# Kernel tuning notes

Measured on AMD Instinct MI355X. Metric: run time of the kernel, lower is better.

## Reference

```python
import jax, jax.numpy as jnp
import numpy as np

N = 16384      # number of nodes (pos rows)
S = 16384      # number of src nodes (src_pos rows)
E = 262144     # number of edges (COO entries)
D = 512        # embed_dim
H = 8          # num_heads
HD = D // H    # head_dim = 64
HID = 1024     # mlp hidden
MLP_IN = D + 3 * H  # 536
EPS = 1e-5


def layer_norm(x, g, b):
    mu = jnp.mean(x, axis=-1, keepdims=True)
    var = jnp.mean((x - mu) ** 2, axis=-1, keepdims=True)
    return (x - mu) * jax.lax.rsqrt(var + EPS) * g + b


def setup_inputs() -> dict:
    key = jax.random.key(0)
    ks = jax.random.split(key, 20)
    s = 1.0 / np.sqrt(D)
    sh = 1.0 / np.sqrt(HID)
    return {
        "x": jax.random.normal(ks[0], (N, D), jnp.float32),
        "Wq": jax.random.uniform(ks[1], (D, D), jnp.float32, -s, s),
        "bq": jnp.zeros((D,), jnp.float32),
        "Wk": jax.random.uniform(ks[2], (D, D), jnp.float32, -s, s),
        "bk": jnp.zeros((D,), jnp.float32),
        "g_att": jnp.ones((D,), jnp.float32),
        "b_att": jnp.zeros((D,), jnp.float32),
        "g_mlp": jnp.ones((D,), jnp.float32),
        "b_mlp": jnp.zeros((D,), jnp.float32),
        "W_in": jax.random.uniform(ks[3], (HID, MLP_IN), jnp.float32, -s, s),
        "b_in": jnp.zeros((HID,), jnp.float32),
        "W_out": jax.random.uniform(ks[4], (D, HID), jnp.float32, -sh, sh),
        "b_out": jnp.zeros((D,), jnp.float32),
        "att_bias": jax.random.normal(ks[5], (H, E), jnp.float32),
        "dist": jax.random.uniform(ks[6], (E,), jnp.float32, 0.5, 6.0),
        "pos": jax.random.normal(ks[7], (N, 3), jnp.float32),
        "src_pos": jax.random.normal(ks[8], (S, 3), jnp.float32),
        "row_index": jax.random.randint(ks[9], (E,), 0, N),
        "src_index": jax.random.randint(ks[10], (E,), 0, S),
        "org_to_src": jax.random.randint(ks[11], (S,), 0, N),
    }


def reference(x, Wq, bq, Wk, bk, g_att, b_att, g_mlp, b_mlp, W_in, b_in,
              W_out, b_out, att_bias, dist, pos, src_pos,
              row_index, src_index, org_to_src):
    n = x.shape[0]
    z = layer_norm(x, g_att, b_att)
    q = (z @ Wq.T + bq).reshape(n, H, HD)          # [N,H,hd]
    k = (z @ Wk.T + bk).reshape(n, H, HD)          # [N,H,hd]
    k_src = k[org_to_src]                          # [S,H,hd]
    # per-edge masked logits: q[row] . k_src[col] / sqrt(hd) + bias
    qe = q[row_index]                              # [E,H,hd]
    ke = k_src[src_index]                          # [E,H,hd]
    logits = jnp.einsum('ehd,ehd->eh', qe, ke) / jnp.sqrt(jnp.float32(HD))
    logits = logits + att_bias.T                   # [E,H]
    # segment (per-row) softmax over incident edges
    m = jax.ops.segment_max(logits, row_index, num_segments=n)
    p = jnp.exp(logits - m[row_index])
    den = jax.ops.segment_sum(p, row_index, num_segments=n)
    att = p / den[row_index]                       # [E,H]
    inv = jnp.where(dist == 0, 0.0, 1.0 / dist)[:, None]
    att = att * inv
    # sparse bmm: feat[h,row] += att * src_pos[col]; rowsum for centering
    sp = src_pos[src_index]                        # [E,3]
    feat = jax.ops.segment_sum(att[:, :, None] * sp[:, None, :],
                               row_index, num_segments=n)   # [N,H,3]
    rowsum = jax.ops.segment_sum(att, row_index, num_segments=n)  # [N,H]
    feat = feat - rowsum[:, :, None] * pos[:, None, :]
    feat = feat.reshape(n, H * 3)
    z2 = layer_norm(x, g_mlp, b_mlp)
    h = jax.nn.gelu(jnp.concatenate([z2, feat], axis=-1) @ W_in.T + b_in)
    return x + (h @ W_out.T + b_out)
```

## Files before the change

### kernel.cpp

```cpp
#include <hip/hip_runtime.h>
#include <math.h>


typedef unsigned short u16;
typedef __attribute__((ext_vector_type(8))) short bf16x8;
typedef __attribute__((ext_vector_type(4))) float f32x4;
typedef __attribute__((ext_vector_type(2))) float f32x2;

constexpr int N_NODES = 16384;
constexpr int E_EDGES = 262144;
constexpr int D = 512;
constexpr int KIN = 544;

constexpr size_t OFF_ZATT = 0;
constexpr size_t OFF_ZCAT = 16777216;
constexpr size_t OFF_WQK  = 34603008;
constexpr size_t OFF_BQK  = 35651584;
constexpr size_t OFF_WIN  = 35655680;
constexpr size_t OFF_WOUT = 36769792;
constexpr size_t OFF_QK   = 37818368;
constexpr size_t OFF_CNT  = 54595584;
constexpr size_t OFF_BKT  = 54661120;
constexpr size_t OFF_ATT  = 58855424;
constexpr size_t OFF_HBF  = 107548672;

static __device__ __forceinline__ u16 f2bf(float f) {
  union { float f; unsigned int u; } v; v.f = f;
  unsigned int u = v.u;
  u = u + 0x7FFFu + ((u >> 16) & 1u);
  return (u16)(u >> 16);
}
static __device__ __forceinline__ void gload16(const u16* g, u16* l) {
  __builtin_amdgcn_global_load_lds(
      (const __attribute__((address_space(1))) unsigned int*)g,
      (__attribute__((address_space(3))) unsigned int*)l, 16, 0, 0);
}

__global__ __launch_bounds__(256) void prep_weights(
    const float* __restrict__ Wq, const float* __restrict__ Wk,
    const float* __restrict__ bq, const float* __restrict__ bk,
    const float* __restrict__ W_in, const float* __restrict__ W_out,
    u16* __restrict__ wqk, float* __restrict__ bqk,
    u16* __restrict__ win, u16* __restrict__ wout)
{
  const int gid = blockIdx.x * 256 + threadIdx.x;
  if (gid < 512 * 1024) {
    wqk[gid]  = f2bf(gid < 512 * 512 ? Wq[gid] : Wk[gid - 512 * 512]);
    wout[gid] = f2bf(W_out[gid]);
  }
  if (gid < 1024 * 544) {
    const int r = gid / 544, c = gid - r * 544;
    win[gid] = f2bf(c < 536 ? W_in[r * 536 + c] : 0.f);
  }
  if (gid < 1024) bqk[gid] = gid < 512 ? bq[gid] : bk[gid - 512];
}

__global__ __launch_bounds__(256) void ln_kernel(
    const float* __restrict__ x,
    const float* __restrict__ g1, const float* __restrict__ b1,
    const float* __restrict__ g2, const float* __restrict__ b2,
    u16* __restrict__ zatt, u16* __restrict__ zcat)
{
  const int row = blockIdx.x;
  const int t = threadIdx.x;
  const float2 v = *(const float2*)(x + (size_t)row * D + t * 2);
  float s = v.x + v.y;
  float s2 = v.x * v.x + v.y * v.y;
#pragma unroll
  for (int m = 1; m < 64; m <<= 1) {
    s  += __shfl_xor(s, m, 64);
    s2 += __shfl_xor(s2, m, 64);
  }
  __shared__ float red[8];
  const int wv = t >> 6;
  if ((t & 63) == 0) { red[wv] = s; red[4 + wv] = s2; }
  __syncthreads();
  s  = red[0] + red[1] + red[2] + red[3];
  s2 = red[4] + red[5] + red[6] + red[7];
  const float mu = s * (1.f / D);
  const float var = s2 * (1.f / D) - mu * mu;
  const float rs = rsqrtf(var + 1e-5f);
  const int c0 = t * 2;
  const float n0 = (v.x - mu) * rs, n1 = (v.y - mu) * rs;
  zatt[(size_t)row * D + c0]       = f2bf(n0 * g1[c0] + b1[c0]);
  zatt[(size_t)row * D + c0 + 1]   = f2bf(n1 * g1[c0 + 1] + b1[c0 + 1]);
  zcat[(size_t)row * KIN + c0]     = f2bf(n0 * g2[c0] + b2[c0]);
  zcat[(size_t)row * KIN + c0 + 1] = f2bf(n1 * g2[c0 + 1] + b2[c0 + 1]);
  if (t < 32) zcat[(size_t)row * KIN + D + t] = 0;
}

__global__ __launch_bounds__(256) void scatter_kernel(
    const int* __restrict__ row_index, int* __restrict__ cnt, int* __restrict__ bucket)
{
  const int gid = blockIdx.x * 256 + threadIdx.x;
  const int r = row_index[gid];
  const int p = atomicAdd(&cnt[r], 1);
  if (p < 64) bucket[(size_t)r * 64 + p] = gid;
}

__global__ __launch_bounds__(256) void tbias_kernel(
    const float* __restrict__ att_bias, float* __restrict__ attT)
{
  const int e = blockIdx.x * 256 + threadIdx.x;
  float v[8];
#pragma unroll
  for (int h = 0; h < 8; ++h) v[h] = att_bias[(size_t)h * E_EDGES + e];
  float* out = attT + (size_t)e * 8;
  *(float4*)out       = *(float4*)&v[0];
  *(float4*)(out + 4) = *(float4*)&v[4];
}

template <int EPI, int WPE>
__global__ __launch_bounds__(256, WPE) void gemm_nt(
    const u16* __restrict__ A, const u16* __restrict__ B,
    const float* __restrict__ bias, const float* __restrict__ resid,
    void* __restrict__ Cout, int M, int Nn, int K)
{
  constexpr int BM = 128, BN = 128, BK = 32;
  __shared__ __align__(16) u16 As[BM * BK];
  __shared__ __align__(16) u16 Bs[BN * BK];
  const int tid = threadIdx.x;
  const int lane = tid & 63;
  const int wave = tid >> 6;
  const int m0 = blockIdx.x * BM;
  const int n0 = blockIdx.y * BN;
  const int wm = (wave >> 1) * 64;
  const int wn = (wave & 1) * 64;
  const int fr = lane & 15;
  const int fq = lane >> 4;
  const int srow = lane >> 2;
  const int skoff = (lane & 3) * 8;

  f32x4 acc[4][4];
#pragma unroll
  for (int i = 0; i < 4; ++i)
#pragma unroll
    for (int j = 0; j < 4; ++j) acc[i][j] = 0.f;

  for (int k0 = 0; k0 < K; k0 += BK) {
    __syncthreads();
#pragma unroll
    for (int r = 0; r < 2; ++r) {
      const int rowbase = r * 64 + wave * 16;
      gload16(A + (size_t)(m0 + rowbase + srow) * K + k0 + skoff, As + rowbase * BK);
      gload16(B + (size_t)(n0 + rowbase + srow) * K + k0 + skoff, Bs + rowbase * BK);
    }
    __syncthreads();
    bf16x8 af[4], bfr[4];
#pragma unroll
    for (int mi = 0; mi < 4; ++mi)
      af[mi] = *(const bf16x8*)(As + (wm + mi * 16 + fr) * BK + fq * 8);
#pragma unroll
    for (int ni = 0; ni < 4; ++ni)
      bfr[ni] = *(const bf16x8*)(Bs + (wn + ni * 16 + fr) * BK + fq * 8);
#pragma unroll
    for (int mi = 0; mi < 4; ++mi)
#pragma unroll
      for (int ni = 0; ni < 4; ++ni)
        acc[mi][ni] = __builtin_amdgcn_mfma_f32_16x16x32_bf16(af[mi], bfr[ni], acc[mi][ni], 0, 0, 0);
  }

#pragma unroll
  for (int mi = 0; mi < 4; ++mi) {
#pragma unroll
    for (int ni = 0; ni < 4; ++ni) {
      const int col = n0 + wn + ni * 16 + fr;
      const float bv = bias[col];
#pragma unroll
      for (int rr = 0; rr < 4; ++rr) {
        const int row = m0 + wm + mi * 16 + fq * 4 + rr;
        float v = acc[mi][ni][rr] + bv;
        if (EPI == 1) {
          const float nu = -1.5957691216057308f * (v + 0.044715f * v * v * v);
          const float sg = __builtin_amdgcn_rcpf(1.f + __expf(nu));
          ((u16*)Cout)[(size_t)row * Nn + col] = f2bf(v * sg);
        } else if (EPI == 2) {
          ((float*)Cout)[(size_t)row * Nn + col] = v + resid[(size_t)row * Nn + col];
        } else {
          const int pk = __builtin_amdgcn_cvt_pk_fp8_f32(v, v, 0, false);
          ((unsigned char*)Cout)[(size_t)row * Nn + col] = (unsigned char)(pk & 0xFF);
        }
      }
    }
  }
}

__global__ __launch_bounds__(256) void edge_csr(
    const unsigned char* __restrict__ qk8, const float* __restrict__ attT,
    const float* __restrict__ dist, const float* __restrict__ src_pos,
    const int* __restrict__ src_index, const int* __restrict__ org_to_src,
    const int* __restrict__ cnt, const int* __restrict__ bucket,
    const float* __restrict__ pos, u16* __restrict__ zcat)
{
  const int lane = threadIdx.x & 63;
  const int wave = threadIdx.x >> 6;
  const int row = blockIdx.x * 4 + wave;
  const int half = lane >> 5;
  const int sub = lane & 31;
  const int h = sub >> 2, j = sub & 3;
  const int deg = cnt[row];
  const int base = row * 64;

  const uint4 qv = *(const uint4*)(qk8 + (size_t)row * 1024 + sub * 16);
  float qf[16];
  {
    const unsigned int* qu = (const unsigned int*)&qv;
#pragma unroll
    for (int i = 0; i < 4; ++i) {
      const f32x2 lo = __builtin_amdgcn_cvt_pk_f32_fp8(qu[i], false);
      const f32x2 hi = __builtin_amdgcn_cvt_pk_f32_fp8(qu[i], true);
      qf[i * 4 + 0] = lo.x; qf[i * 4 + 1] = lo.y;
      qf[i * 4 + 2] = hi.x; qf[i * 4 + 3] = hi.y;
    }
  }

  float accA = 0.f, accB = 0.f;
  const int npair = (deg + 1) >> 1;

  int idx = half;
  bool ok = idx < deg;
  int e = ok ? bucket[base + idx] : 0;
  int s = src_index[e];
  int kr = org_to_src[s];
  uint4 kv = *(const uint4*)(qk8 + (size_t)kr * 1024 + 512 + sub * 16);

  for (int i = 0; i < npair; ++i) {
    const int idx2 = idx + 2;
    const bool ok2 = idx2 < deg;
    const int e2 = ok2 ? bucket[base + idx2] : 0;
    const int s2 = src_index[e2];
    const int kr2 = org_to_src[s2];
    const uint4 kv2 = *(const uint4*)(qk8 + (size_t)kr2 * 1024 + 512 + sub * 16);

    const float bias_h = attT[(size_t)e * 8 + h];
    const float dv = dist[e];
    const float spA = (j >= 2) ? src_pos[(size_t)s * 3 + (j - 2)] : 0.f;
    const float spB = (j == 1) ? src_pos[(size_t)s * 3 + 2] : 0.f;
    float p;
    {
      const unsigned int* ku = (const unsigned int*)&kv;
      const f32x2 a0 = __builtin_amdgcn_cvt_pk_f32_fp8(ku[0], false);
      const f32x2 a1 = __builtin_amdgcn_cvt_pk_f32_fp8(ku[0], true);
      const f32x2 b0 = __builtin_amdgcn_cvt_pk_f32_fp8(ku[1], false);
      const f32x2 b1 = __builtin_amdgcn_cvt_pk_f32_fp8(ku[1], true);
      const f32x2 c0 = __builtin_amdgcn_cvt_pk_f32_fp8(ku[2], false);
      const f32x2 c1 = __builtin_amdgcn_cvt_pk_f32_fp8(ku[2], true);
      const f32x2 d0 = __builtin_amdgcn_cvt_pk_f32_fp8(ku[3], false);
      const f32x2 d1 = __builtin_amdgcn_cvt_pk_f32_fp8(ku[3], true);
      p = qf[0] * a0.x;
      p = fmaf(qf[1],  a0.y, p);  p = fmaf(qf[2],  a1.x, p);  p = fmaf(qf[3],  a1.y, p);
      p = fmaf(qf[4],  b0.x, p);  p = fmaf(qf[5],  b0.y, p);  p = fmaf(qf[6],  b1.x, p);
      p = fmaf(qf[7],  b1.y, p);  p = fmaf(qf[8],  c0.x, p);  p = fmaf(qf[9],  c0.y, p);
      p = fmaf(qf[10], c1.x, p);  p = fmaf(qf[11], c1.y, p);  p = fmaf(qf[12], d0.x, p);
      p = fmaf(qf[13], d0.y, p);  p = fmaf(qf[14], d1.x, p);  p = fmaf(qf[15], d1.y, p);
    }
    p += __shfl_xor(p, 1, 64);
    p += __shfl_xor(p, 2, 64);
    float pe = __expf(p * 0.125f + bias_h);
    pe = ok ? pe : 0.f;
    const float w = (dv == 0.f) ? 0.f : pe / dv;
    accA += (j == 0) ? pe : (j == 1) ? w : w * spA;
    accB += w * spB;

    idx = idx2; ok = ok2; e = e2; s = s2; kv = kv2;
  }

  accA += __shfl_xor(accA, 32, 64);
  accB += __shfl_xor(accB, 32, 64);
  const int hb = h << 2;
  const float den  = __shfl(accA, hb + 0, 64);
  const float wsum = __shfl(accA, hb + 1, 64);
  const float wsp01 = __shfl(accA, hb + 2 + (j & 1), 64);
  const float wsp2  = __shfl(accB, hb + 1, 64);
  const float invd = (den != 0.f) ? 1.f / den : 0.f;
  const float rsum = wsum * invd;
  if (half == 0 && j < 3) {
    const float wspj = (j < 2) ? wsp01 : wsp2;
    zcat[(size_t)row * KIN + D + h * 3 + j] = f2bf(wspj * invd - rsum * pos[row * 3 + j]);
  }
}

extern "C" void kernel_launch(void* const* d_in, const int* in_sizes, int n_in,
                              void* d_out, int out_size, void* d_ws, size_t ws_size,
                              hipStream_t stream)
{
  const float* x        = (const float*)d_in[0];
  const float* Wq       = (const float*)d_in[1];
  const float* bq       = (const float*)d_in[2];
  const float* Wk       = (const float*)d_in[3];
  const float* bk       = (const float*)d_in[4];
  const float* g_att    = (const float*)d_in[5];
  const float* b_att    = (const float*)d_in[6];
  const float* g_mlp    = (const float*)d_in[7];
  const float* b_mlp    = (const float*)d_in[8];
  const float* W_in     = (const float*)d_in[9];
  const float* b_in     = (const float*)d_in[10];
  const float* W_out    = (const float*)d_in[11];
  const float* b_out    = (const float*)d_in[12];
  const float* att_bias = (const float*)d_in[13];
  const float* dist     = (const float*)d_in[14];
  const float* pos      = (const float*)d_in[15];
  const float* src_pos  = (const float*)d_in[16];
  const int* row_index  = (const int*)d_in[17];
  const int* src_index  = (const int*)d_in[18];
  const int* org_to_src = (const int*)d_in[19];

  char* ws = (char*)d_ws;
  u16*   zatt = (u16*)(ws + OFF_ZATT);
  u16*   zcat = (u16*)(ws + OFF_ZCAT);
  u16*   wqk  = (u16*)(ws + OFF_WQK);
  float* bqk  = (float*)(ws + OFF_BQK);
  u16*   win  = (u16*)(ws + OFF_WIN);
  u16*   wout = (u16*)(ws + OFF_WOUT);
  unsigned char* qk8 = (unsigned char*)(ws + OFF_QK);
  int*   cnt  = (int*)(ws + OFF_CNT);
  int*   bkt  = (int*)(ws + OFF_BKT);
  float* attT = (float*)(ws + OFF_ATT);
  u16*   hbf  = (u16*)(ws + OFF_HBF);

  hipMemsetAsync(ws + OFF_CNT, 0, 65536, stream);

  prep_weights<<<2176, 256, 0, stream>>>(Wq, Wk, bq, bk, W_in, W_out, wqk, bqk, win, wout);
  scatter_kernel<<<E_EDGES / 256, 256, 0, stream>>>(row_index, cnt, bkt);
  tbias_kernel<<<E_EDGES / 256, 256, 0, stream>>>(att_bias, attT);
  ln_kernel<<<N_NODES, 256, 0, stream>>>(x, g_att, b_att, g_mlp, b_mlp, zatt, zcat);
  gemm_nt<4, 4><<<dim3(128, 8), 256, 0, stream>>>(zatt, wqk, bqk, nullptr, qk8, N_NODES, 1024, 512);
  edge_csr<<<N_NODES / 4, 256, 0, stream>>>(qk8, attT, dist, src_pos, src_index,
                                            org_to_src, cnt, bkt, pos, zcat);
  gemm_nt<1, 4><<<dim3(128, 8), 256, 0, stream>>>(zcat, win, b_in, nullptr, hbf, N_NODES, 1024, KIN);
  gemm_nt<2, 2><<<dim3(128, 4), 256, 0, stream>>>(hbf, wout, b_out, x, d_out, N_NODES, 512, 1024);
}
```

Baseline: 291.4 us.

## Fuse edge bucketing into weight prep, drop bias transpose, deepen GEMM K-step

Moves the row-bucketing scatter into the weight-prep kernel and removes the separate att_bias transpose kernel, so edge_csr reads att_bias in its original head-major layout. This cuts two launches and a 8MB transpose round-trip, at the cost of strided bias reads. The GEMM now loads two BK=32 slabs per barrier pair (BK effectively 64), halving syncs, which needs K padded to 576 (a multiple of 64) and doubles the LDS footprint. It also clamps the degree at 64 to match bucket capacity.

```diff
diff --git a/kernel.cpp b/kernel.cpp
--- a/kernel.cpp
+++ b/kernel.cpp
@@ -10,19 +10,18 @@
 constexpr int N_NODES = 16384;
 constexpr int E_EDGES = 262144;
 constexpr int D = 512;
-constexpr int KIN = 544;
+constexpr int KIN = 576;
 
 constexpr size_t OFF_ZATT = 0;
 constexpr size_t OFF_ZCAT = 16777216;
-constexpr size_t OFF_WQK  = 34603008;
-constexpr size_t OFF_BQK  = 35651584;
-constexpr size_t OFF_WIN  = 35655680;
-constexpr size_t OFF_WOUT = 36769792;
-constexpr size_t OFF_QK   = 37818368;
-constexpr size_t OFF_CNT  = 54595584;
-constexpr size_t OFF_BKT  = 54661120;
-constexpr size_t OFF_ATT  = 58855424;
-constexpr size_t OFF_HBF  = 107548672;
+constexpr size_t OFF_WQK  = 35651584;
+constexpr size_t OFF_BQK  = 36700160;
+constexpr size_t OFF_WIN  = 36704256;
+constexpr size_t OFF_WOUT = 37883904;
+constexpr size_t OFF_QK   = 38932480;
+constexpr size_t OFF_CNT  = 55709696;
+constexpr size_t OFF_BKT  = 55775232;
+constexpr size_t OFF_HBF  = 59969536;
 
 static __device__ __forceinline__ u16 f2bf(float f) {
   union { float f; unsigned int u; } v; v.f = f;
@@ -40,19 +39,26 @@
     const float* __restrict__ Wq, const float* __restrict__ Wk,
     const float* __restrict__ bq, const float* __restrict__ bk,
     const float* __restrict__ W_in, const float* __restrict__ W_out,
+    const int* __restrict__ row_index,
     u16* __restrict__ wqk, float* __restrict__ bqk,
-    u16* __restrict__ win, u16* __restrict__ wout)
+    u16* __restrict__ win, u16* __restrict__ wout,
+    int* __restrict__ cnt, int* __restrict__ bucket)
 {
   const int gid = blockIdx.x * 256 + threadIdx.x;
   if (gid < 512 * 1024) {
     wqk[gid]  = f2bf(gid < 512 * 512 ? Wq[gid] : Wk[gid - 512 * 512]);
     wout[gid] = f2bf(W_out[gid]);
   }
-  if (gid < 1024 * 544) {
-    const int r = gid / 544, c = gid - r * 544;
+  if (gid < 1024 * KIN) {
+    const int r = gid / KIN, c = gid - r * KIN;
     win[gid] = f2bf(c < 536 ? W_in[r * 536 + c] : 0.f);
   }
   if (gid < 1024) bqk[gid] = gid < 512 ? bq[gid] : bk[gid - 512];
+  if (gid < E_EDGES) {
+    const int r = row_index[gid];
+    const int p = atomicAdd(&cnt[r], 1);
+    if (p < 64) bucket[(size_t)r * 64 + p] = gid;
+  }
 }
 
 __global__ __launch_bounds__(256) void ln_kernel(
@@ -86,28 +92,7 @@
   zatt[(size_t)row * D + c0 + 1]   = f2bf(n1 * g1[c0 + 1] + b1[c0 + 1]);
   zcat[(size_t)row * KIN + c0]     = f2bf(n0 * g2[c0] + b2[c0]);
   zcat[(size_t)row * KIN + c0 + 1] = f2bf(n1 * g2[c0 + 1] + b2[c0 + 1]);
-  if (t < 32) zcat[(size_t)row * KIN + D + t] = 0;
-}
-
-__global__ __launch_bounds__(256) void scatter_kernel(
-    const int* __restrict__ row_index, int* __restrict__ cnt, int* __restrict__ bucket)
-{
-  const int gid = blockIdx.x * 256 + threadIdx.x;
-  const int r = row_index[gid];
-  const int p = atomicAdd(&cnt[r], 1);
-  if (p < 64) bucket[(size_t)r * 64 + p] = gid;
-}
-
-__global__ __launch_bounds__(256) void tbias_kernel(
-    const float* __restrict__ att_bias, float* __restrict__ attT)
-{
-  const int e = blockIdx.x * 256 + threadIdx.x;
-  float v[8];
-#pragma unroll
-  for (int h = 0; h < 8; ++h) v[h] = att_bias[(size_t)h * E_EDGES + e];
-  float* out = attT + (size_t)e * 8;
-  *(float4*)out       = *(float4*)&v[0];
-  *(float4*)(out + 4) = *(float4*)&v[4];
+  if (t < 64) zcat[(size_t)row * KIN + D + t] = 0;
 }
 
 template <int EPI, int WPE>
@@ -117,8 +102,8 @@
     void* __restrict__ Cout, int M, int Nn, int K)
 {
   constexpr int BM = 128, BN = 128, BK = 32;
-  __shared__ __align__(16) u16 As[BM * BK];
-  __shared__ __align__(16) u16 Bs[BN * BK];
+  __shared__ __align__(16) u16 As[2 * BM * BK];
+  __shared__ __align__(16) u16 Bs[2 * BN * BK];
   const int tid = threadIdx.x;
   const int lane = tid & 63;
   const int wave = tid >> 6;
@@ -137,27 +122,35 @@
 #pragma unroll
     for (int j = 0; j < 4; ++j) acc[i][j] = 0.f;
 
-  for (int k0 = 0; k0 < K; k0 += BK) {
+  for (int k0 = 0; k0 < K; k0 += 2 * BK) {
     __syncthreads();
 #pragma unroll
-    for (int r = 0; r < 2; ++r) {
-      const int rowbase = r * 64 + wave * 16;
-      gload16(A + (size_t)(m0 + rowbase + srow) * K + k0 + skoff, As + rowbase * BK);
-      gload16(B + (size_t)(n0 + rowbase + srow) * K + k0 + skoff, Bs + rowbase * BK);
+    for (int t = 0; t < 2; ++t) {
+#pragma unroll
+      for (int r = 0; r < 2; ++r) {
+        const int rowbase = r * 64 + wave * 16;
+        gload16(A + (size_t)(m0 + rowbase + srow) * K + k0 + t * BK + skoff,
+                As + t * (BM * BK) + rowbase * BK);
+        gload16(B + (size_t)(n0 + rowbase + srow) * K + k0 + t * BK + skoff,
+                Bs + t * (BN * BK) + rowbase * BK);
+      }
     }
     __syncthreads();
-    bf16x8 af[4], bfr[4];
-#pragma unroll
-    for (int mi = 0; mi < 4; ++mi)
-      af[mi] = *(const bf16x8*)(As + (wm + mi * 16 + fr) * BK + fq * 8);
-#pragma unroll
-    for (int ni = 0; ni < 4; ++ni)
-      bfr[ni] = *(const bf16x8*)(Bs + (wn + ni * 16 + fr) * BK + fq * 8);
-#pragma unroll
-    for (int mi = 0; mi < 4; ++mi)
+#pragma unroll
+    for (int t = 0; t < 2; ++t) {
+      bf16x8 af[4], bfr[4];
+#pragma unroll
+      for (int mi = 0; mi < 4; ++mi)
+        af[mi] = *(const bf16x8*)(As + t * (BM * BK) + (wm + mi * 16 + fr) * BK + fq * 8);
 #pragma unroll
       for (int ni = 0; ni < 4; ++ni)
-        acc[mi][ni] = __builtin_amdgcn_mfma_f32_16x16x32_bf16(af[mi], bfr[ni], acc[mi][ni], 0, 0, 0);
+        bfr[ni] = *(const bf16x8*)(Bs + t * (BN * BK) + (wn + ni * 16 + fr) * BK + fq * 8);
+#pragma unroll
+      for (int mi = 0; mi < 4; ++mi)
+#pragma unroll
+        for (int ni = 0; ni < 4; ++ni)
+          acc[mi][ni] = __builtin_amdgcn_mfma_f32_16x16x32_bf16(af[mi], bfr[ni], acc[mi][ni], 0, 0, 0);
+    }
   }
 
 #pragma unroll
@@ -186,7 +179,7 @@
 }
 
 __global__ __launch_bounds__(256) void edge_csr(
-    const unsigned char* __restrict__ qk8, const float* __restrict__ attT,
+    const unsigned char* __restrict__ qk8, const float* __restrict__ att_bias,
     const float* __restrict__ dist, const float* __restrict__ src_pos,
     const int* __restrict__ src_index, const int* __restrict__ org_to_src,
     const int* __restrict__ cnt, const int* __restrict__ bucket,
@@ -198,7 +191,7 @@
   const int half = lane >> 5;
   const int sub = lane & 31;
   const int h = sub >> 2, j = sub & 3;
-  const int deg = cnt[row];
+  const int deg = min(cnt[row], 64);
   const int base = row * 64;
 
   const uint4 qv = *(const uint4*)(qk8 + (size_t)row * 1024 + sub * 16);
@@ -232,7 +225,7 @@
     const int kr2 = org_to_src[s2];
     const uint4 kv2 = *(const uint4*)(qk8 + (size_t)kr2 * 1024 + 512 + sub * 16);
 
-    const float bias_h = attT[(size_t)e * 8 + h];
+    const float bias_h = att_bias[(size_t)h * E_EDGES + e];
     const float dv = dist[e];
     const float spA = (j >= 2) ? src_pos[(size_t)s * 3 + (j - 2)] : 0.f;
     const float spB = (j == 1) ? src_pos[(size_t)s * 3 + 2] : 0.f;
@@ -315,17 +308,15 @@
   unsigned char* qk8 = (unsigned char*)(ws + OFF_QK);
   int*   cnt  = (int*)(ws + OFF_CNT);
   int*   bkt  = (int*)(ws + OFF_BKT);
-  float* attT = (float*)(ws + OFF_ATT);
   u16*   hbf  = (u16*)(ws + OFF_HBF);
 
   hipMemsetAsync(ws + OFF_CNT, 0, 65536, stream);
 
-  prep_weights<<<2176, 256, 0, stream>>>(Wq, Wk, bq, bk, W_in, W_out, wqk, bqk, win, wout);
-  scatter_kernel<<<E_EDGES / 256, 256, 0, stream>>>(row_index, cnt, bkt);
-  tbias_kernel<<<E_EDGES / 256, 256, 0, stream>>>(att_bias, attT);
+  prep_weights<<<2304, 256, 0, stream>>>(Wq, Wk, bq, bk, W_in, W_out, row_index,
+                                         wqk, bqk, win, wout, cnt, bkt);
   ln_kernel<<<N_NODES, 256, 0, stream>>>(x, g_att, b_att, g_mlp, b_mlp, zatt, zcat);
   gemm_nt<4, 4><<<dim3(128, 8), 256, 0, stream>>>(zatt, wqk, bqk, nullptr, qk8, N_NODES, 1024, 512);
-  edge_csr<<<N_NODES / 4, 256, 0, stream>>>(qk8, attT, dist, src_pos, src_index,
+  edge_csr<<<N_NODES / 4, 256, 0, stream>>>(qk8, att_bias, dist, src_pos, src_index,
                                             org_to_src, cnt, bkt, pos, zcat);
   gemm_nt<1, 4><<<dim3(128, 8), 256, 0, stream>>>(zcat, win, b_in, nullptr, hbf, N_NODES, 1024, KIN);
   gemm_nt<2, 2><<<dim3(128, 4), 256, 0, stream>>>(hbf, wout, b_out, x, d_out, N_NODES, 512, 1024);
```

New measurement: 289.7 us. Within noise of the previous version (-0.6%).
